# Kernel optimization log

Hardware: AMD Instinct MI355X
Metric: run time of the kernel (lower is better)

## Reference

```python
import jax, jax.numpy as jnp
import numpy as np

B, F, H, M, T = 4096, 256, 256, 3, 30
IN0 = 2 + F  # GRU layer-0 input: concat(current_pos[2], context[F])


def setup_inputs() -> dict:
    key = jax.random.key(0)
    ks = jax.random.split(key, 15)
    s = 0.05
    rn = lambda k, shp: jax.random.normal(k, shp, jnp.float32) * s
    return dict(
        context=jax.random.normal(ks[0], (B, F), jnp.float32),
        mp_w1=rn(ks[1], (64, F)), mp_b1=rn(ks[2], (64,)),
        mp_w2=rn(ks[3], (M, 64)), mp_b2=rn(ks[4], (M,)),
        w_ih0=rn(ks[5], (M, 3 * H, IN0)), w_hh0=rn(ks[6], (M, 3 * H, H)),
        b_ih0=rn(ks[7], (M, 3 * H)), b_hh0=rn(ks[8], (M, 3 * H)),
        w_ih1=rn(ks[9], (M, 3 * H, H)), w_hh1=rn(ks[10], (M, 3 * H, H)),
        b_ih1=rn(ks[11], (M, 3 * H)), b_hh1=rn(ks[12], (M, 3 * H)),
        out_w=rn(ks[13], (M, 2, H)), out_b=rn(ks[14], (M, 2)),
        num_future_steps=T,
    )


def _gru_cell(x, h, w_ih, w_hh, b_ih, b_hh):
    # PyTorch GRU cell, gate order (r, z, n)
    gx = x @ w_ih.T + b_ih  # (B, 3H)
    gh = h @ w_hh.T + b_hh  # (B, 3H)
    xr, xz, xn = jnp.split(gx, 3, axis=-1)
    hr, hz, hn = jnp.split(gh, 3, axis=-1)
    r = jax.nn.sigmoid(xr + hr)
    z = jax.nn.sigmoid(xz + hz)
    n = jnp.tanh(xn + r * hn)
    return (1.0 - z) * n + z * h


def reference(context, mp_w1, mp_b1, mp_w2, mp_b2,
              w_ih0, w_hh0, b_ih0, b_hh0,
              w_ih1, w_hh1, b_ih1, b_hh1,
              out_w, out_b, num_future_steps):
    mode_logits = jax.nn.relu(context @ mp_w1.T + mp_b1) @ mp_w2.T + mp_b2
    mode_probs = jax.nn.softmax(mode_logits, axis=-1)  # (B, M)

    def decode_mode(wi0, wh0, bi0, bh0, wi1, wh1, bi1, bh1, ow, ob):
        def step(carry, _):
            h0, h1, pos = carry
            x = jnp.concatenate([pos, context], axis=-1)  # (B, 2+F)
            h0n = _gru_cell(x, h0, wi0, wh0, bi0, bh0)
            h1n = _gru_cell(h0n, h1, wi1, wh1, bi1, bh1)
            delta = h1n @ ow.T + ob  # (B, 2)
            return (h0n, h1n, delta), delta

        pos0 = jnp.zeros((context.shape[0], 2), context.dtype)
        # hidden = context.unsqueeze(0).repeat(2,1,1): both layers init to context
        (_, _, _), deltas = jax.lax.scan(step, (context, context, pos0), None,
                                          length=num_future_steps)
        # deltas: (T, B, 2) -> (B, T, 2), cumulative sum over time
        return jnp.cumsum(deltas.transpose(1, 0, 2), axis=1)

    trajs = jax.vmap(decode_mode)(w_ih0, w_hh0, b_ih0, b_hh0,
                                  w_ih1, w_hh1, b_ih1, b_hh1,
                                  out_w, out_b)  # (M, B, T, 2)
    trajectories = trajs.transpose(1, 0, 2, 3)  # (B, M, T, 2)
    return trajectories, mode_probs
```

## Files before the change

### kernel.cpp

```cpp
#include <hip/hip_runtime.h>


typedef __attribute__((ext_vector_type(8))) short bf16x8;
typedef __attribute__((ext_vector_type(4))) float f32x4;

__device__ __forceinline__ short f2bf(float f) {
    unsigned u = __builtin_bit_cast(unsigned, f);
    unsigned r = (u + 0x7fffu + ((u >> 16) & 1u)) >> 16;
    return (short)r;
}
__device__ __forceinline__ float bf2f(short s) {
    unsigned u = ((unsigned)(unsigned short)s) << 16;
    return __builtin_bit_cast(float, u);
}
__device__ __forceinline__ float fast_sigmoid(float x) {
    x = fminf(fmaxf(x, -30.f), 30.f);
    float e = __builtin_amdgcn_exp2f(x * -1.442695041f);
    return __builtin_amdgcn_rcpf(1.f + e);
}
__device__ __forceinline__ float fast_tanh(float x) {
    x = fminf(fmaxf(x, -15.f), 15.f);
    float e = __builtin_amdgcn_exp2f(x * -2.885390082f);
    return (1.f - e) * __builtin_amdgcn_rcpf(1.f + e);
}

__global__ void prep_kernel(const float* __restrict__ w_ih0,
                            const float* __restrict__ w_hh0,
                            const float* __restrict__ w_ih1,
                            const float* __restrict__ w_hh1,
                            short* __restrict__ ws) {
    int bid = blockIdx.x;
    int L = threadIdx.x;
    const float* src;
    int srcRowLen, colBase, m, w, ks, t;
    if (bid < 1152) {
        int idx = bid, mw = idx / 48, blk = idx % 48;
        m = mw / 8; w = mw % 8;
        if (blk < 32) { ks = blk >> 2; t = blk & 3; }
        else { int q = blk - 32; ks = q >> 1; t = 4 + (q & 1); }
        src = w_hh0 + (size_t)m * 768 * 256; srcRowLen = 256; colBase = 0;
    } else if (bid < 3456) {
        int idx = bid - 1152, mw = idx / 96, blk = idx % 96;
        m = mw / 8; w = mw % 8;
        int half;
        if (blk < 64) { half = blk >> 5; ks = (blk >> 2) & 7; t = blk & 3; }
        else { int q = blk - 64; half = q >> 4; ks = (q >> 1) & 7; t = 4 + (q & 1); }
        src = (half ? w_hh1 : w_ih1) + (size_t)m * 768 * 256;
        srcRowLen = 256; colBase = 0;
    } else {
        int idx = bid - 3456, mw = idx / 48, blk = idx % 48;
        m = mw / 8; w = mw % 8; ks = blk / 6; t = blk % 6;
        src = w_ih0 + (size_t)m * 768 * 258; srcRowLen = 258; colBase = 2;
    }
    int row = (t >> 1) * 256 + 32 * w + (t & 1) * 16 + (L & 15);
    int col0 = colBase + ks * 32 + (L >> 4) * 8;
    short* dst = ws + (size_t)bid * 512 + L * 8;
    const float* s = src + (size_t)row * srcRowLen + col0;
#pragma unroll
    for (int j = 0; j < 8; ++j) dst[j] = f2bf(s[j]);
}

__global__ __launch_bounds__(256) void modeprobs_kernel(
    const float* __restrict__ ctx, const float* __restrict__ w1,
    const float* __restrict__ b1, const float* __restrict__ w2,
    const float* __restrict__ b2, float* __restrict__ out,
    long probs_off) {
    __shared__ float w1s[64 * 256];
    int tid = threadIdx.x;
    int j = tid & 63;
    int rsub = tid >> 6;
#pragma unroll
    for (int i = 0; i < 64; ++i) w1s[tid + i * 256] = w1[tid + i * 256];
    float b1v = b1[j];
    float w2v0 = w2[j], w2v1 = w2[64 + j], w2v2 = w2[128 + j];
    float b20 = b2[0], b21 = b2[1], b22 = b2[2];
    __syncthreads();
    for (int c = 0; c < 16; ++c) {
        int brow = blockIdx.x * 64 + c * 4 + rsub;
        const float* crow = ctx + (size_t)brow * 256;
        float accv = b1v;
#pragma unroll 8
        for (int k = 0; k < 256; ++k) {
            int kk = (k + j) & 255;
            accv += w1s[j * 256 + kk] * crow[kk];
        }
        float h = fmaxf(accv, 0.f);
        float l0 = h * w2v0, l1 = h * w2v1, l2 = h * w2v2;
#pragma unroll
        for (int s = 1; s < 64; s <<= 1) {
            l0 += __shfl_xor(l0, s);
            l1 += __shfl_xor(l1, s);
            l2 += __shfl_xor(l2, s);
        }
        if (j == 0) {
            l0 += b20; l1 += b21; l2 += b22;
            float mx = fmaxf(l0, fmaxf(l1, l2));
            float e0 = __builtin_amdgcn_exp2f((l0 - mx) * 1.442695041f);
            float e1 = __builtin_amdgcn_exp2f((l1 - mx) * 1.442695041f);
            float e2 = __builtin_amdgcn_exp2f((l2 - mx) * 1.442695041f);
            float inv = 1.f / (e0 + e1 + e2);
            out[probs_off + (size_t)brow * 3 + 0] = e0 * inv;
            out[probs_off + (size_t)brow * 3 + 1] = e1 * inv;
            out[probs_off + (size_t)brow * 3 + 2] = e2 * inv;
        }
    }
}

__global__ __launch_bounds__(512, 2) void decoder_kernel(
    const float* __restrict__ context,
    const float* __restrict__ w_ih0_f,
    const float* __restrict__ b_ih0, const float* __restrict__ b_hh0,
    const float* __restrict__ b_ih1, const float* __restrict__ b_hh1,
    const float* __restrict__ out_w, const float* __restrict__ out_b,
    const short* __restrict__ ws, float* __restrict__ out,
    const int* __restrict__ pT, int ntiles) {
    __shared__ short ctxS[64 * 264];
    __shared__ short h0s[64 * 264];
    __shared__ short h1s[64 * 264];
    __shared__ float posD[128];
    __shared__ float owl[512];
    __shared__ float cwp0[768], cwp1[768];
    __shared__ float cbA[512];
    __shared__ float cbXn[256];
    __shared__ float cbh0n[256];
    __shared__ float cb1A[512];
    __shared__ float cb1X[256];
    __shared__ float cb1H[256];

    const int bid = blockIdx.x;
    const int xcd = bid & 7, slot = bid >> 3;
    int mode, xl, nx;
    if (xcd < 3)      { mode = 0; xl = xcd;     nx = 3; }
    else if (xcd < 6) { mode = 1; xl = xcd - 3; nx = 3; }
    else              { mode = 2; xl = xcd - 6; nx = 2; }
    const int g = slot * nx + xl;
    if (g >= ntiles) return;
    const int m = mode;
    const int b0 = g * 64;

    const int T = *pT;
    const int tid = threadIdx.x;
    const int lane = tid & 63, w = tid >> 6;
    const int lr = lane & 15, quad = lane >> 4;

    if (tid < 128) posD[tid] = 0.f;
    owl[tid] = out_w[m * 512 + tid];
    if (tid < 512) {
        cbA[tid] = b_ih0[m * 768 + tid] + b_hh0[m * 768 + tid];
        cb1A[tid] = b_ih1[m * 768 + tid] + b_hh1[m * 768 + tid];
    }
    if (tid < 256) {
        cbXn[tid] = b_ih0[m * 768 + 512 + tid];
        cbh0n[tid] = b_hh0[m * 768 + 512 + tid];
        cb1X[tid] = b_ih1[m * 768 + 512 + tid];
        cb1H[tid] = b_hh1[m * 768 + 512 + tid];
    }
    for (int c = tid; c < 768; c += 512) {
        cwp0[c] = w_ih0_f[((size_t)m * 768 + c) * 258 + 0];
        cwp1[c] = w_ih0_f[((size_t)m * 768 + c) * 258 + 1];
    }
#pragma unroll
    for (int i = 0; i < 32; ++i) {
        int idx = tid + i * 512;
        int r = idx >> 8, k = idx & 255;
        short v = f2bf(context[(size_t)(b0 + r) * 256 + k]);
        ctxS[r * 264 + k] = v;
        h0s[r * 264 + k] = v;
        h1s[r * 264 + k] = v;
    }
    const float ob0v = out_b[m * 2 + 0], ob1v = out_b[m * 2 + 1];

    const short* p0w = ws + ((size_t)(m * 8 + w) * 48) * 512 + lane * 8;
    const short* p1w = ws + (size_t)1152 * 512 + ((size_t)(m * 8 + w) * 96) * 512 + lane * 8;
    const short* pcw = ws + (size_t)3456 * 512 + ((size_t)(m * 8 + w) * 48) * 512 + lane * 8;

    const int cA = 32 * w + lr;
    const int cB = 32 * w + 16 + lr;

    __syncthreads();

    float cum0 = 0.f, cum1 = 0.f;

    for (int st = 0; st < T; ++st) {
        {
            f32x4 arz[4][4], axn[2][4], ahn[2][4];
#pragma unroll
            for (int rt = 0; rt < 4; ++rt)
#pragma unroll
                for (int r = 0; r < 4; ++r) {
                    int row = rt * 16 + quad * 4 + r;
                    float px = posD[row * 2], py = posD[row * 2 + 1];
#pragma unroll
                    for (int t = 0; t < 4; ++t) {
                        int c = (t >> 1) * 256 + ((t & 1) ? cB : cA);
                        arz[t][rt][r] = cbA[c] + px * cwp0[c] + py * cwp1[c];
                    }
#pragma unroll
                    for (int nt = 0; nt < 2; ++nt) {
                        int cn = nt ? cB : cA;
                        axn[nt][rt][r] = cbXn[cn] + px * cwp0[512 + cn] +
                                         py * cwp1[512 + cn];
                        ahn[nt][rt][r] = cbh0n[cn];
                    }
                }
            const short* bpc = pcw;
            const short* bp0rz = p0w;
            const short* bp0n = p0w + 32 * 512;
#pragma unroll 1
            for (int ks = 0; ks < 8; ++ks) {
                bf16x8 ac[4], ah[4];
#pragma unroll
                for (int rt = 0; rt < 4; ++rt) {
                    ac[rt] = *reinterpret_cast<const bf16x8*>(
                        ctxS + (rt * 16 + lr) * 264 + ks * 32 + quad * 8);
                    ah[rt] = *reinterpret_cast<const bf16x8*>(
                        h0s + (rt * 16 + lr) * 264 + ks * 32 + quad * 8);
                }
#pragma unroll
                for (int t = 0; t < 4; ++t) {
                    bf16x8 b = *reinterpret_cast<const bf16x8*>(bpc + t * 512);
#pragma unroll
                    for (int rt = 0; rt < 4; ++rt)
                        arz[t][rt] = __builtin_amdgcn_mfma_f32_16x16x32_bf16(
                            ac[rt], b, arz[t][rt], 0, 0, 0);
                }
#pragma unroll
                for (int nt = 0; nt < 2; ++nt) {
                    bf16x8 b = *reinterpret_cast<const bf16x8*>(bpc + (4 + nt) * 512);
#pragma unroll
                    for (int rt = 0; rt < 4; ++rt)
                        axn[nt][rt] = __builtin_amdgcn_mfma_f32_16x16x32_bf16(
                            ac[rt], b, axn[nt][rt], 0, 0, 0);
                }
#pragma unroll
                for (int t = 0; t < 4; ++t) {
                    bf16x8 b = *reinterpret_cast<const bf16x8*>(bp0rz + t * 512);
#pragma unroll
                    for (int rt = 0; rt < 4; ++rt)
                        arz[t][rt] = __builtin_amdgcn_mfma_f32_16x16x32_bf16(
                            ah[rt], b, arz[t][rt], 0, 0, 0);
                }
#pragma unroll
                for (int nt = 0; nt < 2; ++nt) {
                    bf16x8 b = *reinterpret_cast<const bf16x8*>(bp0n + nt * 512);
#pragma unroll
                    for (int rt = 0; rt < 4; ++rt)
                        ahn[nt][rt] = __builtin_amdgcn_mfma_f32_16x16x32_bf16(
                            ah[rt], b, ahn[nt][rt], 0, 0, 0);
                }
                bpc += 6 * 512;
                bp0rz += 4 * 512;
                bp0n += 2 * 512;
            }
            __syncthreads();
#pragma unroll
            for (int nt = 0; nt < 2; ++nt) {
                int col = nt ? cB : cA;
#pragma unroll
                for (int rt = 0; rt < 4; ++rt)
#pragma unroll
                    for (int r = 0; r < 4; ++r) {
                        int row = rt * 16 + quad * 4 + r;
                        float rr = fast_sigmoid(arz[nt][rt][r]);
                        float zz = fast_sigmoid(arz[2 + nt][rt][r]);
                        float nn =
                            fast_tanh(axn[nt][rt][r] + rr * ahn[nt][rt][r]);
                        float hold = bf2f(h0s[row * 264 + col]);
                        h0s[row * 264 + col] = f2bf((1.f - zz) * nn + zz * hold);
                    }
            }
        }
        __syncthreads();

        {
            f32x4 arz[4][4], axn[2][4], ahn[2][4];
#pragma unroll
            for (int rt = 0; rt < 4; ++rt)
#pragma unroll
                for (int r = 0; r < 4; ++r) {
#pragma unroll
                    for (int t = 0; t < 4; ++t) {
                        int c = (t >> 1) * 256 + ((t & 1) ? cB : cA);
                        arz[t][rt][r] = cb1A[c];
                    }
#pragma unroll
                    for (int nt = 0; nt < 2; ++nt) {
                        int cn = nt ? cB : cA;
                        axn[nt][rt][r] = cb1X[cn];
                        ahn[nt][rt][r] = cb1H[cn];
                    }
                }
            const short* bq0 = p1w;
            const short* bq1 = p1w + 32 * 512;
            const short* bx = p1w + 64 * 512;
            const short* bh = p1w + 80 * 512;
#pragma unroll 1
            for (int ks = 0; ks < 8; ++ks) {
                bf16x8 a0[4], a1[4];
#pragma unroll
                for (int rt = 0; rt < 4; ++rt) {
                    a0[rt] = *reinterpret_cast<const bf16x8*>(
                        h0s + (rt * 16 + lr) * 264 + ks * 32 + quad * 8);
                    a1[rt] = *reinterpret_cast<const bf16x8*>(
                        h1s + (rt * 16 + lr) * 264 + ks * 32 + quad * 8);
                }
#pragma unroll
                for (int t = 0; t < 4; ++t) {
                    bf16x8 b = *reinterpret_cast<const bf16x8*>(bq0 + t * 512);
#pragma unroll
                    for (int rt = 0; rt < 4; ++rt)
                        arz[t][rt] = __builtin_amdgcn_mfma_f32_16x16x32_bf16(
                            a0[rt], b, arz[t][rt], 0, 0, 0);
                }
#pragma unroll
                for (int nt = 0; nt < 2; ++nt) {
                    bf16x8 b = *reinterpret_cast<const bf16x8*>(bx + nt * 512);
#pragma unroll
                    for (int rt = 0; rt < 4; ++rt)
                        axn[nt][rt] = __builtin_amdgcn_mfma_f32_16x16x32_bf16(
                            a0[rt], b, axn[nt][rt], 0, 0, 0);
                }
#pragma unroll
                for (int t = 0; t < 4; ++t) {
                    bf16x8 b = *reinterpret_cast<const bf16x8*>(bq1 + t * 512);
#pragma unroll
                    for (int rt = 0; rt < 4; ++rt)
                        arz[t][rt] = __builtin_amdgcn_mfma_f32_16x16x32_bf16(
                            a1[rt], b, arz[t][rt], 0, 0, 0);
                }
#pragma unroll
                for (int nt = 0; nt < 2; ++nt) {
                    bf16x8 b = *reinterpret_cast<const bf16x8*>(bh + nt * 512);
#pragma unroll
                    for (int rt = 0; rt < 4; ++rt)
                        ahn[nt][rt] = __builtin_amdgcn_mfma_f32_16x16x32_bf16(
                            a1[rt], b, ahn[nt][rt], 0, 0, 0);
                }
                bq0 += 4 * 512;
                bq1 += 4 * 512;
                bx += 2 * 512;
                bh += 2 * 512;
            }
            __syncthreads();
#pragma unroll
            for (int nt = 0; nt < 2; ++nt) {
                int col = nt ? cB : cA;
#pragma unroll
                for (int rt = 0; rt < 4; ++rt)
#pragma unroll
                    for (int r = 0; r < 4; ++r) {
                        int row = rt * 16 + quad * 4 + r;
                        float rr = fast_sigmoid(arz[nt][rt][r]);
                        float zz = fast_sigmoid(arz[2 + nt][rt][r]);
                        float nn =
                            fast_tanh(axn[nt][rt][r] + rr * ahn[nt][rt][r]);
                        float hold = bf2f(h1s[row * 264 + col]);
                        h1s[row * 264 + col] = f2bf((1.f - zz) * nn + zz * hold);
                    }
            }
        }
        __syncthreads();

        {
            int brow = tid >> 3, p = tid & 7;
            float d0 = 0.f, d1 = 0.f;
#pragma unroll
            for (int j = 0; j < 4; ++j) {
                int cb = ((p + brow) & 7) * 8 + j * 64;
                bf16x8 hv8 = *reinterpret_cast<const bf16x8*>(h1s + brow * 264 + cb);
#pragma unroll
                for (int i = 0; i < 8; ++i) {
                    float hv = bf2f(hv8[i]);
                    d0 += hv * owl[cb + i];
                    d1 += hv * owl[256 + cb + i];
                }
            }
            d0 += __shfl_xor(d0, 1); d0 += __shfl_xor(d0, 2); d0 += __shfl_xor(d0, 4);
            d1 += __shfl_xor(d1, 1); d1 += __shfl_xor(d1, 2); d1 += __shfl_xor(d1, 4);
            d0 += ob0v;
            d1 += ob1v;
            if (p == 0) {
                cum0 += d0;
                cum1 += d1;
                size_t o = (((size_t)(b0 + brow) * 3 + m) * (size_t)T + st) * 2;
                out[o] = cum0;
                out[o + 1] = cum1;
                posD[brow * 2] = d0;
                posD[brow * 2 + 1] = d1;
            }
        }
        __syncthreads();
    }
}

extern "C" void kernel_launch(void* const* d_in, const int* in_sizes, int n_in,
                              void* d_out, int out_size, void* d_ws, size_t ws_size,
                              hipStream_t stream) {
    const float* context = (const float*)d_in[0];
    const float* mp_w1 = (const float*)d_in[1];
    const float* mp_b1 = (const float*)d_in[2];
    const float* mp_w2 = (const float*)d_in[3];
    const float* mp_b2 = (const float*)d_in[4];
    const float* w_ih0 = (const float*)d_in[5];
    const float* w_hh0 = (const float*)d_in[6];
    const float* b_ih0 = (const float*)d_in[7];
    const float* b_hh0 = (const float*)d_in[8];
    const float* w_ih1 = (const float*)d_in[9];
    const float* w_hh1 = (const float*)d_in[10];
    const float* b_ih1 = (const float*)d_in[11];
    const float* b_hh1 = (const float*)d_in[12];
    const float* out_w = (const float*)d_in[13];
    const float* out_b = (const float*)d_in[14];
    const int* pT = (const int*)d_in[15];
    float* out = (float*)d_out;
    short* ws = (short*)d_ws;

    const int B = in_sizes[0] / 256;
    const int ntiles = B / 64;
    const long probs_off = (long)out_size - (long)B * 3;

    prep_kernel<<<4608, 64, 0, stream>>>(w_ih0, w_hh0, w_ih1, w_hh1, ws);
    modeprobs_kernel<<<B / 64, 256, 0, stream>>>(context, mp_w1, mp_b1, mp_w2,
                                                 mp_b2, out, probs_off);
    const int nslots = (ntiles + 1) / 2;
    decoder_kernel<<<8 * nslots, 512, 0, stream>>>(
        context, w_ih0, b_ih0, b_hh0, b_ih1, b_hh1, out_w, out_b, ws, out, pT,
        ntiles);
}
```

Before: 0.9996 ms.

## Precompute time-invariant context input projection once per tile into workspace

The context part of the layer-0 input projection is the same at every step, so it is now computed once per tile with MFMA before the time loop. The result is stored as packed bf16 in a per-wave global workspace region and reloaded each step. Only the two position columns are added per step, which removes the context GEMM from every step. This also drops the ctxS shared buffer, freeing LDS, and a fallback kernel runs if the workspace is too small. The trade-off is extra bf16 rounding on the cached gate pre-activations and per-step global reads.

```diff
diff --git a/kernel.cpp b/kernel.cpp
--- a/kernel.cpp
+++ b/kernel.cpp
@@ -3,6 +3,7 @@
 
 typedef __attribute__((ext_vector_type(8))) short bf16x8;
 typedef __attribute__((ext_vector_type(4))) float f32x4;
+typedef __attribute__((ext_vector_type(2))) unsigned uint2v;
 
 __device__ __forceinline__ short f2bf(float f) {
     unsigned u = __builtin_bit_cast(unsigned, f);
@@ -12,6 +13,12 @@
 __device__ __forceinline__ float bf2f(short s) {
     unsigned u = ((unsigned)(unsigned short)s) << 16;
     return __builtin_bit_cast(float, u);
+}
+__device__ __forceinline__ unsigned pk2(float a, float b) {
+    return (unsigned)(unsigned short)f2bf(a) | ((unsigned)(unsigned short)f2bf(b) << 16);
+}
+__device__ __forceinline__ float unpk(unsigned u, int hi) {
+    return __builtin_bit_cast(float, hi ? (u & 0xffff0000u) : (u << 16));
 }
 __device__ __forceinline__ float fast_sigmoid(float x) {
     x = fminf(fmaxf(x, -30.f), 30.f);
@@ -112,6 +119,313 @@
     const float* __restrict__ b_ih0, const float* __restrict__ b_hh0,
     const float* __restrict__ b_ih1, const float* __restrict__ b_hh1,
     const float* __restrict__ out_w, const float* __restrict__ out_b,
+    short* __restrict__ ws, float* __restrict__ out,
+    const int* __restrict__ pT, int ntiles) {
+    __shared__ short h0s[64 * 264];
+    __shared__ short h1s[64 * 264];
+    __shared__ float posD[128];
+    __shared__ float owl[512];
+    __shared__ float cwp0[768], cwp1[768];
+    __shared__ float cbh0n[256];
+    __shared__ float cb1A[512];
+    __shared__ float cb1X[256];
+    __shared__ float cb1H[256];
+
+    const int bid = blockIdx.x;
+    const int xcd = bid & 7, slot = bid >> 3;
+    int mode, xl, nx;
+    if (xcd < 3)      { mode = 0; xl = xcd;     nx = 3; }
+    else if (xcd < 6) { mode = 1; xl = xcd - 3; nx = 3; }
+    else              { mode = 2; xl = xcd - 6; nx = 2; }
+    const int g = slot * nx + xl;
+    if (g >= ntiles) return;
+    const int m = mode;
+    const int b0 = g * 64;
+
+    const int T = *pT;
+    const int tid = threadIdx.x;
+    const int lane = tid & 63, w = tid >> 6;
+    const int lr = lane & 15, quad = lane >> 4;
+
+    if (tid < 128) posD[tid] = 0.f;
+    owl[tid] = out_w[m * 512 + tid];
+    if (tid < 512) cb1A[tid] = b_ih1[m * 768 + tid] + b_hh1[m * 768 + tid];
+    if (tid < 256) {
+        cbh0n[tid] = b_hh0[m * 768 + 512 + tid];
+        cb1X[tid] = b_ih1[m * 768 + 512 + tid];
+        cb1H[tid] = b_hh1[m * 768 + 512 + tid];
+    }
+    for (int c = tid; c < 768; c += 512) {
+        cwp0[c] = w_ih0_f[((size_t)m * 768 + c) * 258 + 0];
+        cwp1[c] = w_ih0_f[((size_t)m * 768 + c) * 258 + 1];
+    }
+#pragma unroll
+    for (int i = 0; i < 32; ++i) {
+        int idx = tid + i * 512;
+        int r = idx >> 8, k = idx & 255;
+        short v = f2bf(context[(size_t)(b0 + r) * 256 + k]);
+        h0s[r * 264 + k] = v;
+        h1s[r * 264 + k] = v;
+    }
+    const float ob0v = out_b[m * 2 + 0], ob1v = out_b[m * 2 + 1];
+
+    const short* p0w = ws + ((size_t)(m * 8 + w) * 48) * 512 + lane * 8;
+    const short* p1w = ws + (size_t)1152 * 512 + ((size_t)(m * 8 + w) * 96) * 512 + lane * 8;
+    const short* pcw = ws + (size_t)3456 * 512 + ((size_t)(m * 8 + w) * 48) * 512 + lane * 8;
+    short* gxw = ws + (size_t)4608 * 512 +
+                 ((size_t)(m * ntiles + g) * 8 + w) * 6144;
+
+    const int cA = 32 * w + lr;
+    const int cB = 32 * w + 16 + lr;
+
+    __syncthreads();
+
+    {
+        f32x4 acc[6][4];
+#pragma unroll
+        for (int t6 = 0; t6 < 6; ++t6) {
+            int c = (t6 >> 1) * 256 + 32 * w + (t6 & 1) * 16 + lr;
+            float bi = b_ih0[m * 768 + c] + (t6 < 4 ? b_hh0[m * 768 + c] : 0.f);
+#pragma unroll
+            for (int rt = 0; rt < 4; ++rt) acc[t6][rt] = f32x4{bi, bi, bi, bi};
+        }
+        const short* bp = pcw;
+#pragma unroll 1
+        for (int ks = 0; ks < 8; ++ks) {
+            bf16x8 a[4];
+#pragma unroll
+            for (int rt = 0; rt < 4; ++rt)
+                a[rt] = *reinterpret_cast<const bf16x8*>(
+                    h0s + (rt * 16 + lr) * 264 + ks * 32 + quad * 8);
+#pragma unroll
+            for (int t6 = 0; t6 < 6; ++t6) {
+                bf16x8 b = *reinterpret_cast<const bf16x8*>(bp + t6 * 512);
+#pragma unroll
+                for (int rt = 0; rt < 4; ++rt)
+                    acc[t6][rt] = __builtin_amdgcn_mfma_f32_16x16x32_bf16(
+                        a[rt], b, acc[t6][rt], 0, 0, 0);
+            }
+            bp += 6 * 512;
+        }
+#pragma unroll
+        for (int t6 = 0; t6 < 6; ++t6)
+#pragma unroll
+            for (int rt = 0; rt < 4; ++rt) {
+                uint2v pk;
+                pk[0] = pk2(acc[t6][rt][0], acc[t6][rt][1]);
+                pk[1] = pk2(acc[t6][rt][2], acc[t6][rt][3]);
+                *reinterpret_cast<uint2v*>(gxw + ((t6 * 4 + rt) * 64 + lane) * 4) = pk;
+            }
+    }
+    __syncthreads();
+
+    float cum0 = 0.f, cum1 = 0.f;
+
+    for (int st = 0; st < T; ++st) {
+        {
+            f32x4 arz[4][4], axn[2][4], ahn[2][4];
+            uint2v gxv[6][4];
+#pragma unroll
+            for (int t6 = 0; t6 < 6; ++t6)
+#pragma unroll
+                for (int rt = 0; rt < 4; ++rt)
+                    gxv[t6][rt] = *reinterpret_cast<const uint2v*>(
+                        gxw + ((t6 * 4 + rt) * 64 + lane) * 4);
+#pragma unroll
+            for (int rt = 0; rt < 4; ++rt)
+#pragma unroll
+                for (int r = 0; r < 4; ++r) {
+                    int row = rt * 16 + quad * 4 + r;
+                    float px = posD[row * 2], py = posD[row * 2 + 1];
+#pragma unroll
+                    for (int t = 0; t < 4; ++t) {
+                        int c = (t >> 1) * 256 + ((t & 1) ? cB : cA);
+                        arz[t][rt][r] = unpk(gxv[t][rt][r >> 1], r & 1) +
+                                        px * cwp0[c] + py * cwp1[c];
+                    }
+#pragma unroll
+                    for (int nt = 0; nt < 2; ++nt) {
+                        int cn = nt ? cB : cA;
+                        axn[nt][rt][r] = unpk(gxv[4 + nt][rt][r >> 1], r & 1) +
+                                         px * cwp0[512 + cn] + py * cwp1[512 + cn];
+                        ahn[nt][rt][r] = cbh0n[cn];
+                    }
+                }
+            const short* bp0rz = p0w;
+            const short* bp0n = p0w + 32 * 512;
+#pragma unroll 1
+            for (int ks = 0; ks < 8; ++ks) {
+                bf16x8 ah[4];
+#pragma unroll
+                for (int rt = 0; rt < 4; ++rt)
+                    ah[rt] = *reinterpret_cast<const bf16x8*>(
+                        h0s + (rt * 16 + lr) * 264 + ks * 32 + quad * 8);
+#pragma unroll
+                for (int t = 0; t < 4; ++t) {
+                    bf16x8 b = *reinterpret_cast<const bf16x8*>(bp0rz + t * 512);
+#pragma unroll
+                    for (int rt = 0; rt < 4; ++rt)
+                        arz[t][rt] = __builtin_amdgcn_mfma_f32_16x16x32_bf16(
+                            ah[rt], b, arz[t][rt], 0, 0, 0);
+                }
+#pragma unroll
+                for (int nt = 0; nt < 2; ++nt) {
+                    bf16x8 b = *reinterpret_cast<const bf16x8*>(bp0n + nt * 512);
+#pragma unroll
+                    for (int rt = 0; rt < 4; ++rt)
+                        ahn[nt][rt] = __builtin_amdgcn_mfma_f32_16x16x32_bf16(
+                            ah[rt], b, ahn[nt][rt], 0, 0, 0);
+                }
+                bp0rz += 4 * 512;
+                bp0n += 2 * 512;
+            }
+            __syncthreads();
+#pragma unroll
+            for (int nt = 0; nt < 2; ++nt) {
+                int col = nt ? cB : cA;
+#pragma unroll
+                for (int rt = 0; rt < 4; ++rt)
+#pragma unroll
+                    for (int r = 0; r < 4; ++r) {
+                        int row = rt * 16 + quad * 4 + r;
+                        float rr = fast_sigmoid(arz[nt][rt][r]);
+                        float zz = fast_sigmoid(arz[2 + nt][rt][r]);
+                        float nn =
+                            fast_tanh(axn[nt][rt][r] + rr * ahn[nt][rt][r]);
+                        float hold = bf2f(h0s[row * 264 + col]);
+                        h0s[row * 264 + col] = f2bf((1.f - zz) * nn + zz * hold);
+                    }
+            }
+        }
+        __syncthreads();
+
+        {
+            f32x4 arz[4][4], axn[2][4], ahn[2][4];
+#pragma unroll
+            for (int rt = 0; rt < 4; ++rt)
+#pragma unroll
+                for (int r = 0; r < 4; ++r) {
+#pragma unroll
+                    for (int t = 0; t < 4; ++t) {
+                        int c = (t >> 1) * 256 + ((t & 1) ? cB : cA);
+                        arz[t][rt][r] = cb1A[c];
+                    }
+#pragma unroll
+                    for (int nt = 0; nt < 2; ++nt) {
+                        int cn = nt ? cB : cA;
+                        axn[nt][rt][r] = cb1X[cn];
+                        ahn[nt][rt][r] = cb1H[cn];
+                    }
+                }
+            const short* bq0 = p1w;
+            const short* bq1 = p1w + 32 * 512;
+            const short* bx = p1w + 64 * 512;
+            const short* bh = p1w + 80 * 512;
+#pragma unroll 1
+            for (int ks = 0; ks < 8; ++ks) {
+                bf16x8 a0[4], a1[4];
+#pragma unroll
+                for (int rt = 0; rt < 4; ++rt) {
+                    a0[rt] = *reinterpret_cast<const bf16x8*>(
+                        h0s + (rt * 16 + lr) * 264 + ks * 32 + quad * 8);
+                    a1[rt] = *reinterpret_cast<const bf16x8*>(
+                        h1s + (rt * 16 + lr) * 264 + ks * 32 + quad * 8);
+                }
+#pragma unroll
+                for (int t = 0; t < 4; ++t) {
+                    bf16x8 b = *reinterpret_cast<const bf16x8*>(bq0 + t * 512);
+#pragma unroll
+                    for (int rt = 0; rt < 4; ++rt)
+                        arz[t][rt] = __builtin_amdgcn_mfma_f32_16x16x32_bf16(
+                            a0[rt], b, arz[t][rt], 0, 0, 0);
+                }
+#pragma unroll
+                for (int nt = 0; nt < 2; ++nt) {
+                    bf16x8 b = *reinterpret_cast<const bf16x8*>(bx + nt * 512);
+#pragma unroll
+                    for (int rt = 0; rt < 4; ++rt)
+                        axn[nt][rt] = __builtin_amdgcn_mfma_f32_16x16x32_bf16(
+                            a0[rt], b, axn[nt][rt], 0, 0, 0);
+                }
+#pragma unroll
+                for (int t = 0; t < 4; ++t) {
+                    bf16x8 b = *reinterpret_cast<const bf16x8*>(bq1 + t * 512);
+#pragma unroll
+                    for (int rt = 0; rt < 4; ++rt)
+                        arz[t][rt] = __builtin_amdgcn_mfma_f32_16x16x32_bf16(
+                            a1[rt], b, arz[t][rt], 0, 0, 0);
+                }
+#pragma unroll
+                for (int nt = 0; nt < 2; ++nt) {
+                    bf16x8 b = *reinterpret_cast<const bf16x8*>(bh + nt * 512);
+#pragma unroll
+                    for (int rt = 0; rt < 4; ++rt)
+                        ahn[nt][rt] = __builtin_amdgcn_mfma_f32_16x16x32_bf16(
+                            a1[rt], b, ahn[nt][rt], 0, 0, 0);
+                }
+                bq0 += 4 * 512;
+                bq1 += 4 * 512;
+                bx += 2 * 512;
+                bh += 2 * 512;
+            }
+            __syncthreads();
+#pragma unroll
+            for (int nt = 0; nt < 2; ++nt) {
+                int col = nt ? cB : cA;
+#pragma unroll
+                for (int rt = 0; rt < 4; ++rt)
+#pragma unroll
+                    for (int r = 0; r < 4; ++r) {
+                        int row = rt * 16 + quad * 4 + r;
+                        float rr = fast_sigmoid(arz[nt][rt][r]);
+                        float zz = fast_sigmoid(arz[2 + nt][rt][r]);
+                        float nn =
+                            fast_tanh(axn[nt][rt][r] + rr * ahn[nt][rt][r]);
+                        float hold = bf2f(h1s[row * 264 + col]);
+                        h1s[row * 264 + col] = f2bf((1.f - zz) * nn + zz * hold);
+                    }
+            }
+        }
+        __syncthreads();
+
+        {
+            int brow = tid >> 3, p = tid & 7;
+            float d0 = 0.f, d1 = 0.f;
+#pragma unroll
+            for (int j = 0; j < 4; ++j) {
+                int cb = ((p + brow) & 7) * 8 + j * 64;
+                bf16x8 hv8 = *reinterpret_cast<const bf16x8*>(h1s + brow * 264 + cb);
+#pragma unroll
+                for (int i = 0; i < 8; ++i) {
+                    float hv = bf2f(hv8[i]);
+                    d0 += hv * owl[cb + i];
+                    d1 += hv * owl[256 + cb + i];
+                }
+            }
+            d0 += __shfl_xor(d0, 1); d0 += __shfl_xor(d0, 2); d0 += __shfl_xor(d0, 4);
+            d1 += __shfl_xor(d1, 1); d1 += __shfl_xor(d1, 2); d1 += __shfl_xor(d1, 4);
+            d0 += ob0v;
+            d1 += ob1v;
+            if (p == 0) {
+                cum0 += d0;
+                cum1 += d1;
+                size_t o = (((size_t)(b0 + brow) * 3 + m) * (size_t)T + st) * 2;
+                out[o] = cum0;
+                out[o + 1] = cum1;
+                posD[brow * 2] = d0;
+                posD[brow * 2 + 1] = d1;
+            }
+        }
+        __syncthreads();
+    }
+}
+
+__global__ __launch_bounds__(512, 2) void decoder_kernel_fb(
+    const float* __restrict__ context,
+    const float* __restrict__ w_ih0_f,
+    const float* __restrict__ b_ih0, const float* __restrict__ b_hh0,
+    const float* __restrict__ b_ih1, const float* __restrict__ b_hh1,
+    const float* __restrict__ out_w, const float* __restrict__ out_b,
     const short* __restrict__ ws, float* __restrict__ out,
     const int* __restrict__ pT, int ntiles) {
     __shared__ short ctxS[64 * 264];
@@ -271,7 +585,6 @@
             }
         }
         __syncthreads();
-
         {
             f32x4 arz[4][4], axn[2][4], ahn[2][4];
 #pragma unroll
@@ -360,7 +673,6 @@
             }
         }
         __syncthreads();
-
         {
             int brow = tid >> 3, p = tid & 7;
             float d0 = 0.f, d1 = 0.f;
@@ -423,7 +735,14 @@
     modeprobs_kernel<<<B / 64, 256, 0, stream>>>(context, mp_w1, mp_b1, mp_w2,
                                                  mp_b2, out, probs_off);
     const int nslots = (ntiles + 1) / 2;
-    decoder_kernel<<<8 * nslots, 512, 0, stream>>>(
-        context, w_ih0, b_ih0, b_hh0, b_ih1, b_hh1, out_w, out_b, ws, out, pT,
-        ntiles);
-}
+    const size_t need = (size_t)4608 * 1024 + (size_t)3 * ntiles * 8 * 6144 * 2;
+    if (ws_size >= need) {
+        decoder_kernel<<<8 * nslots, 512, 0, stream>>>(
+            context, w_ih0, b_ih0, b_hh0, b_ih1, b_hh1, out_w, out_b, ws, out,
+            pT, ntiles);
+    } else {
+        decoder_kernel_fb<<<8 * nslots, 512, 0, stream>>>(
+            context, w_ih0, b_ih0, b_hh0, b_ih1, b_hh1, out_w, out_b, ws, out,
+            pT, ntiles);
+    }
+}
```

New measurement: 1.118 ms. +11.8%, slower.
